# Kernel tuning notes

Hardware: AMD Instinct MI355X
Metric: run time of the kernel (lower is better)

## Reference

```python
import jax, jax.numpy as jnp
import numpy as np

EPS = 1e-5  # torch BatchNorm2d default eps

def _bn(x, gamma, beta):
    # training-mode batch statistics over (N,H,W), per channel (biased variance)
    mean = jnp.mean(x, axis=(0, 2, 3), keepdims=True)
    var = jnp.var(x, axis=(0, 2, 3), keepdims=True)
    return gamma[None, :, None, None] * (x - mean) * jax.lax.rsqrt(var + EPS) + beta[None, :, None, None]

def _conv1x1(x, w, b):
    # (B,C,H,W) x (O,C) -> (B,O,H,W)
    return jnp.einsum('bchw,oc->bohw', x, w) + b[None, :, None, None]

def _maxpool2(x):
    B, C, H, W = x.shape
    return x.reshape(B, C, H // 2, 2, W // 2, 2).max(axis=(3, 5))

def setup_inputs() -> dict:
    key = jax.random.key(0)
    ks = jax.random.split(key, 5)
    B, C, H, W = 16, 256, 56, 56
    Ci, Cg = C // 8, C // 4
    def kaiming(k, o, i):
        return jax.random.normal(k, (o, i), jnp.float32) * np.float32(np.sqrt(2.0 / i))
    return {
        'x': jax.random.normal(ks[0], (B, C, H, W), jnp.float32),
        'bn1_gamma': jnp.ones((C,), jnp.float32),
        'bn1_beta': jnp.zeros((C,), jnp.float32),
        'w_g': kaiming(ks[1], Cg, C), 'b_g': jnp.zeros((Cg,), jnp.float32),
        'w_theta': kaiming(ks[2], Ci, C), 'b_theta': jnp.zeros((Ci,), jnp.float32),
        'w_phi': kaiming(ks[3], Ci, C), 'b_phi': jnp.zeros((Ci,), jnp.float32),
        'bn2_gamma': jnp.ones((Cg,), jnp.float32),
        'bn2_beta': jnp.zeros((Cg,), jnp.float32),
        'w_z': kaiming(ks[4], C, Cg), 'b_z': jnp.zeros((C,), jnp.float32),
    }

def reference(x, bn1_gamma, bn1_beta, w_g, b_g, w_theta, b_theta, w_phi, b_phi, bn2_gamma, bn2_beta, w_z, b_z):
    identity = x
    B, C, H, W = x.shape
    xa = jax.nn.relu(_bn(x, bn1_gamma, bn1_beta))
    g_x = _maxpool2(_conv1x1(xa, w_g, b_g))        # (B,Cg,H/2,W/2)
    phi_x = _maxpool2(_conv1x1(xa, w_phi, b_phi))  # (B,Ci,H/2,W/2)
    theta_x = _conv1x1(xa, w_theta, b_theta)       # (B,Ci,H,W)
    Cg = g_x.shape[1]
    Ci = theta_x.shape[1]
    Np = g_x.shape[2] * g_x.shape[3]               # subsampled positions (H/2*W/2)
    g_x = g_x.reshape(B, Cg, Np).transpose(0, 2, 1)      # (B,Np,Cg)
    phi_x = phi_x.reshape(B, Ci, Np)                     # (B,Ci,Np)
    theta_x = theta_x.reshape(B, Ci, H * W).transpose(0, 2, 1)  # (B,HW,Ci)
    f_div_C = jnp.einsum('bnc,bcm->bnm', theta_x, phi_x) / Np   # (B,HW,Np)
    y = jnp.einsum('bnm,bmc->bnc', f_div_C, g_x)                # (B,HW,Cg)
    y = y.transpose(0, 2, 1).reshape(B, Cg, H, W)
    w_y = _conv1x1(jax.nn.relu(_bn(y, bn2_gamma, bn2_beta)), w_z, b_z)
    return w_y + identity
```

## Files before the change

kernel.cpp:

```cpp
#include <hip/hip_runtime.h>
#include <hip/hip_bf16.h>

#define BB 16
#define CC 256
#define HWN 3136
#define NCG 64
#define NCI 32
#define NPP 784

typedef __attribute__((ext_vector_type(8))) short short8;
typedef __attribute__((ext_vector_type(4))) float floatx4;

__device__ __forceinline__ unsigned short f2bf(float f) {
    union { __hip_bfloat16 h; unsigned short u; } cv;
    cv.h = __float2bfloat16(f);
    return cv.u;
}
__device__ __forceinline__ float bf2f(unsigned short u) {
    return __uint_as_float(((unsigned)u) << 16);
}

__global__ __launch_bounds__(256) void k_prep(const float* __restrict__ w_t,
                                              const float* __restrict__ w_p,
                                              const float* __restrict__ w_g,
                                              const float* __restrict__ w_z,
                                              unsigned short* __restrict__ wcat,
                                              unsigned short* __restrict__ wzb,
                                              unsigned short* __restrict__ pool,
                                              float* __restrict__ accs) {
    int o = blockIdx.x;
    int c = threadIdx.x;
    const float* src = (o < 32) ? (w_t + o * CC)
                      : (o < 64) ? (w_p + (o - 32) * CC)
                                 : (w_g + (o - 64) * CC);
    wcat[o * CC + c] = f2bf(src[c]);
    {
        int r = o * 2 + (c >> 7);
        int kk = c & 127;
        if (kk < 72)
            wzb[r * 72 + kk] = (kk < 64) ? f2bf(w_z[r * 64 + kk]) : (unsigned short)0;
    }
    if (o < 96) {
        int b = c >> 4, kk = c & 15;
        pool[((size_t)(b * 96 + o)) * 800 + 784 + kk] = 0;
    }
    if (o == 0) {
        for (int i = c; i < 640; i += 256) accs[i] = 0.f;
    }
}

__global__ __launch_bounds__(256) void k_bn1a(const float* __restrict__ x,
                                              float* __restrict__ acc) {
    int blk = blockIdx.x;
    int c = blk & (CC - 1);
    const float4* p = (const float4*)(x + (size_t)blk * HWN);
    int tid = threadIdx.x;
    float s = 0.f, q = 0.f;
    #pragma unroll
    for (int i = tid; i < 784; i += 256) {
        float4 v = p[i];
        s += v.x + v.y + v.z + v.w;
        q += v.x * v.x + v.y * v.y + v.z * v.z + v.w * v.w;
    }
    #pragma unroll
    for (int off = 32; off > 0; off >>= 1) {
        s += __shfl_down(s, off);
        q += __shfl_down(q, off);
    }
    __shared__ float sh[8];
    int wid = tid >> 6, lane = tid & 63;
    if (lane == 0) { sh[wid] = s; sh[4 + wid] = q; }
    __syncthreads();
    if (tid == 0) {
        atomicAdd(&acc[c], sh[0] + sh[1] + sh[2] + sh[3]);
        atomicAdd(&acc[CC + c], sh[4] + sh[5] + sh[6] + sh[7]);
    }
}

__global__ __launch_bounds__(256) void k_conv1(const float* __restrict__ x,
                                               const unsigned short* __restrict__ wcat,
                                               const float* __restrict__ bn1acc,
                                               const float* __restrict__ gamma,
                                               const float* __restrict__ beta,
                                               const float* __restrict__ b_g,
                                               const float* __restrict__ b_t,
                                               const float* __restrict__ b_p,
                                               unsigned short* __restrict__ th,
                                               unsigned short* __restrict__ pool) {
    int b  = blockIdx.y;
    int bx = blockIdx.x;
    int hw0 = bx * 112;
    int tid = threadIdx.x;
    int wv = tid >> 6, ln = tid & 63;
    int col = ln & 15, quad = ln >> 4;

    __shared__ unsigned short smem[128 * 120];
    unsigned short* As = smem;
    unsigned short* Bs = smem + 4096;
    __shared__ float ab_s[512];
    __shared__ float bias_s[128];

    {
        const float inv = 1.0f / (BB * HWN);
        float mean = bn1acc[tid] * inv;
        float var  = bn1acc[CC + tid] * inv - mean * mean;
        float a = gamma[tid] * rsqrtf(var + 1e-5f);
        ab_s[tid] = a;
        ab_s[CC + tid] = beta[tid] - mean * a;
    }
    if (tid < 128) {
        int o = tid;
        bias_s[o] = (o < 32) ? b_t[o] : (o < 64) ? b_p[o - 32] : b_g[o - 64];
    }
    __syncthreads();

    floatx4 acc[2][7];
    #pragma unroll
    for (int mt = 0; mt < 2; ++mt)
        for (int nt = 0; nt < 7; ++nt)
            acc[mt][nt] = (floatx4){0.f, 0.f, 0.f, 0.f};

    int p   = tid & 15;
    int hwq = tid >> 4;
    const float* xb = x + (size_t)(b * CC) * HWN + hw0;

    for (int k0 = 0; k0 < CC; k0 += 32) {
        #pragma unroll
        for (int i = 0; i < 2; ++i) {
            int row = wv * 32 + i * 16 + (ln >> 2);
            int q   = ln & 3;
            const unsigned short* gp = wcat + row * CC + k0 + q * 8;
            __builtin_amdgcn_global_load_lds(
                (const __attribute__((address_space(1))) unsigned int*)gp,
                (__attribute__((address_space(3))) unsigned int*)&As[(wv * 2 + i) * 512],
                16, 0, 0);
        }
        {
            int c0 = k0 + 2 * p;
            float a0 = ab_s[c0],     d0 = ab_s[CC + c0];
            float a1 = ab_s[c0 + 1], d1 = ab_s[CC + c0 + 1];
            unsigned int* bw = (unsigned int*)Bs;
            #pragma unroll
            for (int t = 0; t < 2; ++t) {
                int qi = hwq + 16 * t;
                if (qi < 28) {
                    float4 v0 = *(const float4*)(xb + (size_t)c0 * HWN + qi * 4);
                    float4 v1 = *(const float4*)(xb + (size_t)(c0 + 1) * HWN + qi * 4);
                    float r0[4] = { fmaxf(fmaf(a0, v0.x, d0), 0.f), fmaxf(fmaf(a0, v0.y, d0), 0.f),
                                    fmaxf(fmaf(a0, v0.z, d0), 0.f), fmaxf(fmaf(a0, v0.w, d0), 0.f) };
                    float r1[4] = { fmaxf(fmaf(a1, v1.x, d1), 0.f), fmaxf(fmaf(a1, v1.y, d1), 0.f),
                                    fmaxf(fmaf(a1, v1.z, d1), 0.f), fmaxf(fmaf(a1, v1.w, d1), 0.f) };
                    #pragma unroll
                    for (int i = 0; i < 4; ++i) {
                        unsigned int w = (unsigned int)f2bf(r0[i]) | ((unsigned int)f2bf(r1[i]) << 16);
                        bw[(qi * 4 + i) * 16 + p] = w;
                    }
                }
            }
        }
        __syncthreads();

        short8 af0 = *(const short8*)&As[(wv * 32 +      col) * 32 + quad * 8];
        short8 af1 = *(const short8*)&As[(wv * 32 + 16 + col) * 32 + quad * 8];
        #pragma unroll
        for (int nt = 0; nt < 7; ++nt) {
            short8 bf = *(const short8*)&Bs[(nt * 16 + col) * 32 + quad * 8];
            acc[0][nt] = __builtin_amdgcn_mfma_f32_16x16x32_bf16(af0, bf, acc[0][nt], 0, 0, 0);
            acc[1][nt] = __builtin_amdgcn_mfma_f32_16x16x32_bf16(af1, bf, acc[1][nt], 0, 0, 0);
        }
        __syncthreads();
    }

    unsigned short* Ct = smem;
    #pragma unroll
    for (int mt = 0; mt < 2; ++mt) {
        int obase = wv * 32 + mt * 16 + quad * 4;
        #pragma unroll
        for (int r = 0; r < 4; ++r) {
            float bias = bias_s[obase + r];
            #pragma unroll
            for (int nt = 0; nt < 7; ++nt)
                Ct[(obase + r) * 120 + nt * 16 + col] = f2bf(acc[mt][nt][r] + bias);
        }
    }
    __syncthreads();

    #pragma unroll
    for (int i = 0; i < 4; ++i) {
        int e = tid + i * 256;
        if (e < 896) {
            int ch = e / 28, c4 = e - ch * 28;
            ushort4 v = *(const ushort4*)&Ct[ch * 120 + c4 * 4];
            *(ushort4*)&th[((size_t)(b * NCI + ch)) * HWN + hw0 + c4 * 4] = v;
        }
    }
    #pragma unroll
    for (int i = 0; i < 11; ++i) {
        int e = tid + i * 256;
        if (e < 2688) {
            int ch = e / 28, m = e - ch * 28;
            const unsigned short* r0p = &Ct[(32 + ch) * 120 + 2 * m];
            float v = fmaxf(fmaxf(bf2f(r0p[0]), bf2f(r0p[1])),
                            fmaxf(bf2f(r0p[56]), bf2f(r0p[57])));
            pool[((size_t)(b * 96 + ch)) * 800 + bx * 28 + m] = f2bf(v);
        }
    }
}

__global__ __launch_bounds__(256) void k_sgemm(const unsigned short* __restrict__ pool,
                                               unsigned short* __restrict__ Sg) {
    int b = blockIdx.x;
    int tid = threadIdx.x;
    int wv = tid >> 6, ln = tid & 63;
    int col = ln & 15, quad = ln >> 4;
    __shared__ float Sred[4 * 2048];

    const unsigned short* gbase = pool + ((size_t)(b * 96 + 32)) * 800;
    const unsigned short* pbase = pool + ((size_t)(b * 96)) * 800;

    floatx4 acc[4][2];
    #pragma unroll
    for (int mt = 0; mt < 4; ++mt)
        for (int nt = 0; nt < 2; ++nt)
            acc[mt][nt] = (floatx4){0.f, 0.f, 0.f, 0.f};

    for (int s = wv; s < 25; s += 4) {
        int k0 = s * 32;
        short8 af[4], bfr[2];
        #pragma unroll
        for (int mt = 0; mt < 4; ++mt)
            af[mt] = *(const short8*)&gbase[(mt * 16 + col) * 800 + k0 + quad * 8];
        #pragma unroll
        for (int nt = 0; nt < 2; ++nt)
            bfr[nt] = *(const short8*)&pbase[(nt * 16 + col) * 800 + k0 + quad * 8];
        #pragma unroll
        for (int mt = 0; mt < 4; ++mt)
            #pragma unroll
            for (int nt = 0; nt < 2; ++nt)
                acc[mt][nt] = __builtin_amdgcn_mfma_f32_16x16x32_bf16(af[mt], bfr[nt], acc[mt][nt], 0, 0, 0);
    }
    #pragma unroll
    for (int mt = 0; mt < 4; ++mt)
        for (int nt = 0; nt < 2; ++nt)
            for (int r = 0; r < 4; ++r) {
                int cg = mt * 16 + quad * 4 + r;
                int ci = nt * 16 + col;
                Sred[wv * 2048 + cg * 32 + ci] = acc[mt][nt][r];
            }
    __syncthreads();
    #pragma unroll
    for (int j = 0; j < 8; ++j) {
        int idx = tid + j * 256;
        float s = Sred[idx] + Sred[2048 + idx] + Sred[4096 + idx] + Sred[6144 + idx];
        int cg = idx >> 5, ci = idx & 31;
        Sg[(size_t)b * 2560 + cg * 40 + ci] = f2bf(s * (1.0f / NPP));
    }
}

__global__ __launch_bounds__(256) void k_y(const unsigned short* __restrict__ th,
                                           const unsigned short* __restrict__ Sg,
                                           unsigned short* __restrict__ y,
                                           float* __restrict__ bn2acc) {
    int b = blockIdx.y;
    int hw0 = blockIdx.x * 64;
    int tid = threadIdx.x;
    int wv = tid >> 6, ln = tid & 63;
    int col = ln & 15, quad = ln >> 4;

    __shared__ unsigned short St[64 * 40];
    __shared__ unsigned short Tt[64 * 40];
    __shared__ float shs[64], shq[64];

    {
        const unsigned int* sgw = (const unsigned int*)(Sg + (size_t)b * 2560);
        unsigned int* stw = (unsigned int*)St;
        for (int i = tid; i < 1280; i += 256) stw[i] = sgw[i];
    }
    {
        int p2 = tid & 15, hwq = tid >> 4;
        int c0 = 2 * p2;
        const unsigned short* tb = th + (size_t)(b * NCI) * HWN + hw0 + hwq * 4;
        ushort4 v0 = *(const ushort4*)(tb + (size_t)c0 * HWN);
        ushort4 v1 = *(const ushort4*)(tb + (size_t)(c0 + 1) * HWN);
        unsigned int* tw = (unsigned int*)Tt;
        tw[(hwq * 4 + 0) * 20 + p2] = (unsigned)v0.x | ((unsigned)v1.x << 16);
        tw[(hwq * 4 + 1) * 20 + p2] = (unsigned)v0.y | ((unsigned)v1.y << 16);
        tw[(hwq * 4 + 2) * 20 + p2] = (unsigned)v0.z | ((unsigned)v1.z << 16);
        tw[(hwq * 4 + 3) * 20 + p2] = (unsigned)v0.w | ((unsigned)v1.w << 16);
    }
    if (tid < 64) { shs[tid] = 0.f; shq[tid] = 0.f; }
    __syncthreads();

    short8 af = *(const short8*)&Tt[(wv * 16 + col) * 40 + quad * 8];
    #pragma unroll
    for (int nt = 0; nt < 4; ++nt) {
        short8 bf = *(const short8*)&St[(nt * 16 + col) * 40 + quad * 8];
        floatx4 acc = (floatx4){0.f, 0.f, 0.f, 0.f};
        acc = __builtin_amdgcn_mfma_f32_16x16x32_bf16(af, bf, acc, 0, 0, 0);
        int cg = nt * 16 + col;
        int hw = hw0 + wv * 16 + quad * 4;
        ushort4 st;
        st.x = f2bf(acc[0]); st.y = f2bf(acc[1]);
        st.z = f2bf(acc[2]); st.w = f2bf(acc[3]);
        *(ushort4*)&y[((size_t)(b * NCG + cg)) * HWN + hw] = st;
        float s = acc[0] + acc[1] + acc[2] + acc[3];
        float q = acc[0] * acc[0] + acc[1] * acc[1] + acc[2] * acc[2] + acc[3] * acc[3];
        atomicAdd(&shs[cg], s);
        atomicAdd(&shq[cg], q);
    }
    __syncthreads();
    if (tid < 64) {
        atomicAdd(&bn2acc[tid], shs[tid]);
        atomicAdd(&bn2acc[64 + tid], shq[tid]);
    }
}

__global__ __launch_bounds__(256) void k_convz(const unsigned short* __restrict__ y,
                                               const unsigned short* __restrict__ wzb,
                                               const float* __restrict__ bn2acc,
                                               const float* __restrict__ gamma,
                                               const float* __restrict__ beta,
                                               const float* __restrict__ b_z,
                                               const float* __restrict__ x,
                                               float* __restrict__ out) {
    int b = blockIdx.y;
    int hw0 = blockIdx.x * 64;
    int tid = threadIdx.x;
    int wv = tid >> 6, ln = tid & 63;
    int col = ln & 15, quad = ln >> 4;

    __shared__ unsigned short Wl[256 * 72];
    __shared__ unsigned short Yt[64 * 72];
    __shared__ float ab2_s[128];

    #pragma unroll
    for (int i = 0; i < 9; ++i) {
        int j = wv * 9 + i;
        const unsigned short* gp = wzb + j * 512 + ln * 8;
        __builtin_amdgcn_global_load_lds(
            (const __attribute__((address_space(1))) unsigned int*)gp,
            (__attribute__((address_space(3))) unsigned int*)&Wl[j * 512],
            16, 0, 0);
    }
    if (tid < 64) {
        const float inv = 1.0f / (BB * HWN);
        float mean = bn2acc[tid] * inv;
        float var  = bn2acc[64 + tid] * inv - mean * mean;
        float a = gamma[tid] * rsqrtf(var + 1e-5f);
        ab2_s[tid] = a;
        ab2_s[64 + tid] = beta[tid] - mean * a;
    }
    __syncthreads();

    {
        int p2 = tid & 15, hwq = tid >> 4;
        const unsigned short* ybase = y + (size_t)(b * NCG) * HWN + hw0 + hwq * 4;
        unsigned int* yw = (unsigned int*)Yt;
        #pragma unroll
        for (int h = 0; h < 2; ++h) {
            int k0 = h * 32 + 2 * p2;
            ushort4 v0 = *(const ushort4*)(ybase + (size_t)k0 * HWN);
            ushort4 v1 = *(const ushort4*)(ybase + (size_t)(k0 + 1) * HWN);
            float a0 = ab2_s[k0],     d0 = ab2_s[64 + k0];
            float a1 = ab2_s[k0 + 1], d1 = ab2_s[64 + k0 + 1];
            float r0[4] = { fmaxf(fmaf(a0, bf2f(v0.x), d0), 0.f), fmaxf(fmaf(a0, bf2f(v0.y), d0), 0.f),
                            fmaxf(fmaf(a0, bf2f(v0.z), d0), 0.f), fmaxf(fmaf(a0, bf2f(v0.w), d0), 0.f) };
            float r1[4] = { fmaxf(fmaf(a1, bf2f(v1.x), d1), 0.f), fmaxf(fmaf(a1, bf2f(v1.y), d1), 0.f),
                            fmaxf(fmaf(a1, bf2f(v1.z), d1), 0.f), fmaxf(fmaf(a1, bf2f(v1.w), d1), 0.f) };
            #pragma unroll
            for (int i = 0; i < 4; ++i) {
                unsigned int w = (unsigned int)f2bf(r0[i]) | ((unsigned int)f2bf(r1[i]) << 16);
                yw[(hwq * 4 + i) * 36 + h * 16 + p2] = w;
            }
        }
    }
    __syncthreads();

    floatx4 acc[16];
    #pragma unroll
    for (int nt = 0; nt < 16; ++nt) acc[nt] = (floatx4){0.f, 0.f, 0.f, 0.f};

    #pragma unroll
    for (int kk = 0; kk < 2; ++kk) {
        short8 af = *(const short8*)&Yt[(wv * 16 + col) * 72 + kk * 32 + quad * 8];
        #pragma unroll
        for (int nt = 0; nt < 16; ++nt) {
            short8 bf = *(const short8*)&Wl[(nt * 16 + col) * 72 + kk * 32 + quad * 8];
            acc[nt] = __builtin_amdgcn_mfma_f32_16x16x32_bf16(af, bf, acc[nt], 0, 0, 0);
        }
    }

    #pragma unroll
    for (int nt = 0; nt < 16; ++nt) {
        int co = nt * 16 + col;
        size_t base = ((size_t)(b * CC + co)) * HWN + hw0 + wv * 16 + quad * 4;
        float4 xv = *(const float4*)&x[base];
        float bz = b_z[co];
        float4 r = make_float4(acc[nt][0] + bz + xv.x, acc[nt][1] + bz + xv.y,
                               acc[nt][2] + bz + xv.z, acc[nt][3] + bz + xv.w);
        *(float4*)&out[base] = r;
    }
}

extern "C" void kernel_launch(void* const* d_in, const int* in_sizes, int n_in,
                              void* d_out, int out_size, void* d_ws, size_t ws_size,
                              hipStream_t stream) {
    (void)in_sizes; (void)n_in; (void)out_size; (void)ws_size;
    const float* x   = (const float*)d_in[0];
    const float* g1  = (const float*)d_in[1];
    const float* b1  = (const float*)d_in[2];
    const float* w_g = (const float*)d_in[3];
    const float* b_g = (const float*)d_in[4];
    const float* w_t = (const float*)d_in[5];
    const float* b_t = (const float*)d_in[6];
    const float* w_p = (const float*)d_in[7];
    const float* b_p = (const float*)d_in[8];
    const float* g2  = (const float*)d_in[9];
    const float* b2  = (const float*)d_in[10];
    const float* w_z = (const float*)d_in[11];
    const float* b_z = (const float*)d_in[12];
    float* out = (float*)d_out;

    float* ws     = (float*)d_ws;
    float* bn1acc = ws;
    float* bn2acc = ws + 512;
    unsigned short* wcat  = (unsigned short*)(ws + 1024);
    unsigned short* wzb   = (unsigned short*)(ws + 17408);
    unsigned short* th    = (unsigned short*)(ws + 26624);
    unsigned short* pool  = (unsigned short*)(ws + 829440);
    unsigned short* Sg    = (unsigned short*)(ws + 1443840);
    unsigned short* yb    = (unsigned short*)(ws + 1464320);

    k_prep  <<<dim3(128),     dim3(256), 0, stream>>>(w_t, w_p, w_g, w_z, wcat, wzb, pool, ws);
    k_bn1a  <<<dim3(BB * CC), dim3(256), 0, stream>>>(x, bn1acc);
    k_conv1 <<<dim3(28, BB),  dim3(256), 0, stream>>>(x, wcat, bn1acc, g1, b1, b_g, b_t, b_p, th, pool);
    k_sgemm <<<dim3(BB),      dim3(256), 0, stream>>>(pool, Sg);
    k_y     <<<dim3(49, BB),  dim3(256), 0, stream>>>(th, Sg, yb, bn2acc);
    k_convz <<<dim3(49, BB),  dim3(256), 0, stream>>>(yb, wzb, bn2acc, g2, b2, b_z, x, out);
}
```

Baseline: 192.8 us.

## Derive BN2 statistics algebraically from theta Gram matrix and fuse y into convz

Instead of materialising y and accumulating its BN2 statistics in a separate kernel, the per-channel sum and sum-of-squares of y are computed from theta row sums and the theta Gram matrix combined with the small S matrix inside k_sgemm. k_y is removed and y is recomputed on the fly in k_convz, which is also split over two output-channel halves. conv1 additionally prefetches the next x chunk into registers. This removes a full write and read of the y tensor, at the cost of extra Gram work in the 16-block sgemm kernel and y being recomputed twice per tile in convz.

```diff
diff --git a/kernel.cpp b/kernel.cpp
--- a/kernel.cpp
+++ b/kernel.cpp
@@ -45,7 +45,7 @@
         pool[((size_t)(b * 96 + o)) * 800 + 784 + kk] = 0;
     }
     if (o == 0) {
-        for (int i = c; i < 640; i += 256) accs[i] = 0.f;
+        for (int i = c; i < 1152; i += 256) accs[i] = 0.f;
     }
 }
 
@@ -86,7 +86,8 @@
                                                const float* __restrict__ b_t,
                                                const float* __restrict__ b_p,
                                                unsigned short* __restrict__ th,
-                                               unsigned short* __restrict__ pool) {
+                                               unsigned short* __restrict__ pool,
+                                               float* __restrict__ T1g) {
     int b  = blockIdx.y;
     int bx = blockIdx.x;
     int hw0 = bx * 112;
@@ -123,6 +124,18 @@
     int p   = tid & 15;
     int hwq = tid >> 4;
     const float* xb = x + (size_t)(b * CC) * HWN + hw0;
+    bool q1 = (hwq + 16) < 28;
+
+    float4 pv0[2], pv1[2];
+    {
+        int c0 = 2 * p;
+        pv0[0] = *(const float4*)(xb + (size_t)c0 * HWN + hwq * 4);
+        pv1[0] = *(const float4*)(xb + (size_t)(c0 + 1) * HWN + hwq * 4);
+        if (q1) {
+            pv0[1] = *(const float4*)(xb + (size_t)c0 * HWN + (hwq + 16) * 4);
+            pv1[1] = *(const float4*)(xb + (size_t)(c0 + 1) * HWN + (hwq + 16) * 4);
+        }
+    }
 
     for (int k0 = 0; k0 < CC; k0 += 32) {
         #pragma unroll
@@ -142,10 +155,9 @@
             unsigned int* bw = (unsigned int*)Bs;
             #pragma unroll
             for (int t = 0; t < 2; ++t) {
-                int qi = hwq + 16 * t;
-                if (qi < 28) {
-                    float4 v0 = *(const float4*)(xb + (size_t)c0 * HWN + qi * 4);
-                    float4 v1 = *(const float4*)(xb + (size_t)(c0 + 1) * HWN + qi * 4);
+                if (t == 0 || q1) {
+                    int qi = hwq + 16 * t;
+                    float4 v0 = pv0[t], v1 = pv1[t];
                     float r0[4] = { fmaxf(fmaf(a0, v0.x, d0), 0.f), fmaxf(fmaf(a0, v0.y, d0), 0.f),
                                     fmaxf(fmaf(a0, v0.z, d0), 0.f), fmaxf(fmaf(a0, v0.w, d0), 0.f) };
                     float r1[4] = { fmaxf(fmaf(a1, v1.x, d1), 0.f), fmaxf(fmaf(a1, v1.y, d1), 0.f),
@@ -158,6 +170,15 @@
                 }
             }
         }
+        if (k0 + 32 < CC) {
+            int c0 = k0 + 32 + 2 * p;
+            pv0[0] = *(const float4*)(xb + (size_t)c0 * HWN + hwq * 4);
+            pv1[0] = *(const float4*)(xb + (size_t)(c0 + 1) * HWN + hwq * 4);
+            if (q1) {
+                pv0[1] = *(const float4*)(xb + (size_t)c0 * HWN + (hwq + 16) * 4);
+                pv1[1] = *(const float4*)(xb + (size_t)(c0 + 1) * HWN + (hwq + 16) * 4);
+            }
+        }
         __syncthreads();
 
         short8 af0 = *(const short8*)&As[(wv * 32 +      col) * 32 + quad * 8];
@@ -193,6 +214,17 @@
             ushort4 v = *(const ushort4*)&Ct[ch * 120 + c4 * 4];
             *(ushort4*)&th[((size_t)(b * NCI + ch)) * HWN + hw0 + c4 * 4] = v;
         }
+    }
+    {
+        int row = tid >> 3;
+        int seg = tid & 7;
+        float s = 0.f;
+        #pragma unroll
+        for (int j = 0; j < 14; ++j) s += bf2f(Ct[row * 120 + seg * 14 + j]);
+        s += __shfl_down(s, 4);
+        s += __shfl_down(s, 2);
+        s += __shfl_down(s, 1);
+        if (seg == 0) atomicAdd(&T1g[b * NCI + row], s);
     }
     #pragma unroll
     for (int i = 0; i < 11; ++i) {
@@ -207,70 +239,153 @@
     }
 }
 
-__global__ __launch_bounds__(256) void k_sgemm(const unsigned short* __restrict__ pool,
-                                               unsigned short* __restrict__ Sg) {
+__global__ __launch_bounds__(512) void k_sgemm(const unsigned short* __restrict__ pool,
+                                               const unsigned short* __restrict__ th,
+                                               const float* __restrict__ T1g,
+                                               unsigned short* __restrict__ Sg,
+                                               float* __restrict__ bn2acc) {
     int b = blockIdx.x;
     int tid = threadIdx.x;
     int wv = tid >> 6, ln = tid & 63;
     int col = ln & 15, quad = ln >> 4;
     __shared__ float Sred[4 * 2048];
-
-    const unsigned short* gbase = pool + ((size_t)(b * 96 + 32)) * 800;
-    const unsigned short* pbase = pool + ((size_t)(b * 96)) * 800;
-
-    floatx4 acc[4][2];
-    #pragma unroll
-    for (int mt = 0; mt < 4; ++mt)
-        for (int nt = 0; nt < 2; ++nt)
-            acc[mt][nt] = (floatx4){0.f, 0.f, 0.f, 0.f};
-
-    for (int s = wv; s < 25; s += 4) {
-        int k0 = s * 32;
-        short8 af[4], bfr[2];
+    __shared__ float Gred[4 * 1024];
+    __shared__ float T1s[32];
+    __shared__ float shs[64], shq[64];
+
+    if (tid < 64) { shs[tid] = 0.f; shq[tid] = 0.f; }
+    if (tid < 32) T1s[tid] = T1g[b * NCI + tid];
+
+    if (wv < 4) {
+        const unsigned short* gbase = pool + ((size_t)(b * 96 + 32)) * 800;
+        const unsigned short* pbase = pool + ((size_t)(b * 96)) * 800;
+        floatx4 acc[4][2];
         #pragma unroll
         for (int mt = 0; mt < 4; ++mt)
-            af[mt] = *(const short8*)&gbase[(mt * 16 + col) * 800 + k0 + quad * 8];
-        #pragma unroll
-        for (int nt = 0; nt < 2; ++nt)
-            bfr[nt] = *(const short8*)&pbase[(nt * 16 + col) * 800 + k0 + quad * 8];
+            for (int nt = 0; nt < 2; ++nt)
+                acc[mt][nt] = (floatx4){0.f, 0.f, 0.f, 0.f};
+        for (int s = wv; s < 25; s += 4) {
+            int k0 = s * 32;
+            short8 af[4], bfr[2];
+            #pragma unroll
+            for (int mt = 0; mt < 4; ++mt)
+                af[mt] = *(const short8*)&gbase[(mt * 16 + col) * 800 + k0 + quad * 8];
+            #pragma unroll
+            for (int nt = 0; nt < 2; ++nt)
+                bfr[nt] = *(const short8*)&pbase[(nt * 16 + col) * 800 + k0 + quad * 8];
+            #pragma unroll
+            for (int mt = 0; mt < 4; ++mt)
+                #pragma unroll
+                for (int nt = 0; nt < 2; ++nt)
+                    acc[mt][nt] = __builtin_amdgcn_mfma_f32_16x16x32_bf16(af[mt], bfr[nt], acc[mt][nt], 0, 0, 0);
+        }
         #pragma unroll
         for (int mt = 0; mt < 4; ++mt)
-            #pragma unroll
             for (int nt = 0; nt < 2; ++nt)
-                acc[mt][nt] = __builtin_amdgcn_mfma_f32_16x16x32_bf16(af[mt], bfr[nt], acc[mt][nt], 0, 0, 0);
-    }
-    #pragma unroll
-    for (int mt = 0; mt < 4; ++mt)
-        for (int nt = 0; nt < 2; ++nt)
-            for (int r = 0; r < 4; ++r) {
-                int cg = mt * 16 + quad * 4 + r;
-                int ci = nt * 16 + col;
-                Sred[wv * 2048 + cg * 32 + ci] = acc[mt][nt][r];
-            }
-    __syncthreads();
-    #pragma unroll
-    for (int j = 0; j < 8; ++j) {
-        int idx = tid + j * 256;
+                for (int r = 0; r < 4; ++r) {
+                    int cg = mt * 16 + quad * 4 + r;
+                    int ci = nt * 16 + col;
+                    Sred[wv * 2048 + cg * 32 + ci] = acc[mt][nt][r];
+                }
+    } else {
+        int gw = wv - 4;
+        const unsigned short* tb = th + (size_t)(b * NCI) * HWN;
+        floatx4 ga[2][2];
+        #pragma unroll
+        for (int m = 0; m < 2; ++m)
+            for (int n = 0; n < 2; ++n)
+                ga[m][n] = (floatx4){0.f, 0.f, 0.f, 0.f};
+        for (int t = gw; t < 98; t += 4) {
+            int k0 = t * 32;
+            short8 a0 = *(const short8*)&tb[(size_t)col * HWN + k0 + quad * 8];
+            short8 a1 = *(const short8*)&tb[(size_t)(16 + col) * HWN + k0 + quad * 8];
+            ga[0][0] = __builtin_amdgcn_mfma_f32_16x16x32_bf16(a0, a0, ga[0][0], 0, 0, 0);
+            ga[0][1] = __builtin_amdgcn_mfma_f32_16x16x32_bf16(a0, a1, ga[0][1], 0, 0, 0);
+            ga[1][0] = __builtin_amdgcn_mfma_f32_16x16x32_bf16(a1, a0, ga[1][0], 0, 0, 0);
+            ga[1][1] = __builtin_amdgcn_mfma_f32_16x16x32_bf16(a1, a1, ga[1][1], 0, 0, 0);
+        }
+        #pragma unroll
+        for (int m = 0; m < 2; ++m)
+            for (int n = 0; n < 2; ++n)
+                for (int r = 0; r < 4; ++r)
+                    Gred[gw * 1024 + (m * 16 + quad * 4 + r) * 32 + n * 16 + col] = ga[m][n][r];
+    }
+    __syncthreads();
+
+    for (int idx = tid; idx < 2048; idx += 512) {
         float s = Sred[idx] + Sred[2048 + idx] + Sred[4096 + idx] + Sred[6144 + idx];
         int cg = idx >> 5, ci = idx & 31;
-        Sg[(size_t)b * 2560 + cg * 40 + ci] = f2bf(s * (1.0f / NPP));
-    }
-}
-
-__global__ __launch_bounds__(256) void k_y(const unsigned short* __restrict__ th,
-                                           const unsigned short* __restrict__ Sg,
-                                           unsigned short* __restrict__ y,
-                                           float* __restrict__ bn2acc) {
+        unsigned short h = f2bf(s * (1.0f / NPP));
+        Sg[(size_t)b * 2560 + cg * 40 + ci] = h;
+        Sred[idx] = bf2f(h);
+    }
+    for (int idx = tid; idx < 1024; idx += 512) {
+        Gred[idx] = Gred[idx] + Gred[1024 + idx] + Gred[2048 + idx] + Gred[3072 + idx];
+    }
+    __syncthreads();
+
+    {
+        int cg = tid & 63, part = tid >> 6;
+        float sum = 0.f, sq = 0.f;
+        #pragma unroll
+        for (int i = 0; i < 4; ++i) {
+            int ci = part * 4 + i;
+            float sv = Sred[cg * 32 + ci];
+            sum += sv * T1s[ci];
+            float t = 0.f;
+            #pragma unroll
+            for (int cj = 0; cj < 32; ++cj)
+                t += Gred[ci * 32 + cj] * Sred[cg * 32 + cj];
+            sq += sv * t;
+        }
+        atomicAdd(&shs[cg], sum);
+        atomicAdd(&shq[cg], sq);
+    }
+    __syncthreads();
+    if (tid < 64) {
+        atomicAdd(&bn2acc[tid], shs[tid]);
+        atomicAdd(&bn2acc[64 + tid], shq[tid]);
+    }
+}
+
+__global__ __launch_bounds__(256) void k_convz(const unsigned short* __restrict__ th,
+                                               const unsigned short* __restrict__ Sg,
+                                               const unsigned short* __restrict__ wzb,
+                                               const float* __restrict__ bn2acc,
+                                               const float* __restrict__ gamma,
+                                               const float* __restrict__ beta,
+                                               const float* __restrict__ b_z,
+                                               const float* __restrict__ x,
+                                               float* __restrict__ out) {
     int b = blockIdx.y;
     int hw0 = blockIdx.x * 64;
+    int coh = blockIdx.z * 128;
     int tid = threadIdx.x;
     int wv = tid >> 6, ln = tid & 63;
     int col = ln & 15, quad = ln >> 4;
 
-    __shared__ unsigned short St[64 * 40];
-    __shared__ unsigned short Tt[64 * 40];
-    __shared__ float shs[64], shq[64];
-
+    __shared__ unsigned short Wl[128 * 72];
+    __shared__ unsigned short TS[5120];
+    __shared__ float ab2_s[128];
+    unsigned short* Tt = TS;
+    unsigned short* St = TS + 2560;
+    unsigned short* Yt = TS;
+
+    for (int j = wv; j < 18; j += 4) {
+        const unsigned short* gp = wzb + coh * 72 + j * 512 + ln * 8;
+        __builtin_amdgcn_global_load_lds(
+            (const __attribute__((address_space(1))) unsigned int*)gp,
+            (__attribute__((address_space(3))) unsigned int*)&Wl[j * 512],
+            16, 0, 0);
+    }
+    if (tid < 64) {
+        const float inv = 1.0f / (BB * HWN);
+        float mean = bn2acc[tid] * inv;
+        float var  = bn2acc[64 + tid] * inv - mean * mean;
+        float a = gamma[tid] * rsqrtf(var + 1e-5f);
+        ab2_s[tid] = a;
+        ab2_s[64 + tid] = beta[tid] - mean * a;
+    }
     {
         const unsigned int* sgw = (const unsigned int*)(Sg + (size_t)b * 2560);
         unsigned int* stw = (unsigned int*)St;
@@ -288,111 +403,47 @@
         tw[(hwq * 4 + 2) * 20 + p2] = (unsigned)v0.z | ((unsigned)v1.z << 16);
         tw[(hwq * 4 + 3) * 20 + p2] = (unsigned)v0.w | ((unsigned)v1.w << 16);
     }
-    if (tid < 64) { shs[tid] = 0.f; shq[tid] = 0.f; }
-    __syncthreads();
-
-    short8 af = *(const short8*)&Tt[(wv * 16 + col) * 40 + quad * 8];
+    __syncthreads();
+
+    short8 afy = *(const short8*)&Tt[(wv * 16 + col) * 40 + quad * 8];
+    floatx4 yacc[4];
     #pragma unroll
     for (int nt = 0; nt < 4; ++nt) {
         short8 bf = *(const short8*)&St[(nt * 16 + col) * 40 + quad * 8];
-        floatx4 acc = (floatx4){0.f, 0.f, 0.f, 0.f};
-        acc = __builtin_amdgcn_mfma_f32_16x16x32_bf16(af, bf, acc, 0, 0, 0);
+        floatx4 z = (floatx4){0.f, 0.f, 0.f, 0.f};
+        yacc[nt] = __builtin_amdgcn_mfma_f32_16x16x32_bf16(afy, bf, z, 0, 0, 0);
+    }
+    __syncthreads();
+
+    #pragma unroll
+    for (int nt = 0; nt < 4; ++nt) {
         int cg = nt * 16 + col;
-        int hw = hw0 + wv * 16 + quad * 4;
-        ushort4 st;
-        st.x = f2bf(acc[0]); st.y = f2bf(acc[1]);
-        st.z = f2bf(acc[2]); st.w = f2bf(acc[3]);
-        *(ushort4*)&y[((size_t)(b * NCG + cg)) * HWN + hw] = st;
-        float s = acc[0] + acc[1] + acc[2] + acc[3];
-        float q = acc[0] * acc[0] + acc[1] * acc[1] + acc[2] * acc[2] + acc[3] * acc[3];
-        atomicAdd(&shs[cg], s);
-        atomicAdd(&shq[cg], q);
-    }
-    __syncthreads();
-    if (tid < 64) {
-        atomicAdd(&bn2acc[tid], shs[tid]);
-        atomicAdd(&bn2acc[64 + tid], shq[tid]);
-    }
-}
-
-__global__ __launch_bounds__(256) void k_convz(const unsigned short* __restrict__ y,
-                                               const unsigned short* __restrict__ wzb,
-                                               const float* __restrict__ bn2acc,
-                                               const float* __restrict__ gamma,
-                                               const float* __restrict__ beta,
-                                               const float* __restrict__ b_z,
-                                               const float* __restrict__ x,
-                                               float* __restrict__ out) {
-    int b = blockIdx.y;
-    int hw0 = blockIdx.x * 64;
-    int tid = threadIdx.x;
-    int wv = tid >> 6, ln = tid & 63;
-    int col = ln & 15, quad = ln >> 4;
-
-    __shared__ unsigned short Wl[256 * 72];
-    __shared__ unsigned short Yt[64 * 72];
-    __shared__ float ab2_s[128];
-
-    #pragma unroll
-    for (int i = 0; i < 9; ++i) {
-        int j = wv * 9 + i;
-        const unsigned short* gp = wzb + j * 512 + ln * 8;
-        __builtin_amdgcn_global_load_lds(
-            (const __attribute__((address_space(1))) unsigned int*)gp,
-            (__attribute__((address_space(3))) unsigned int*)&Wl[j * 512],
-            16, 0, 0);
-    }
-    if (tid < 64) {
-        const float inv = 1.0f / (BB * HWN);
-        float mean = bn2acc[tid] * inv;
-        float var  = bn2acc[64 + tid] * inv - mean * mean;
-        float a = gamma[tid] * rsqrtf(var + 1e-5f);
-        ab2_s[tid] = a;
-        ab2_s[64 + tid] = beta[tid] - mean * a;
-    }
-    __syncthreads();
-
-    {
-        int p2 = tid & 15, hwq = tid >> 4;
-        const unsigned short* ybase = y + (size_t)(b * NCG) * HWN + hw0 + hwq * 4;
-        unsigned int* yw = (unsigned int*)Yt;
-        #pragma unroll
-        for (int h = 0; h < 2; ++h) {
-            int k0 = h * 32 + 2 * p2;
-            ushort4 v0 = *(const ushort4*)(ybase + (size_t)k0 * HWN);
-            ushort4 v1 = *(const ushort4*)(ybase + (size_t)(k0 + 1) * HWN);
-            float a0 = ab2_s[k0],     d0 = ab2_s[64 + k0];
-            float a1 = ab2_s[k0 + 1], d1 = ab2_s[64 + k0 + 1];
-            float r0[4] = { fmaxf(fmaf(a0, bf2f(v0.x), d0), 0.f), fmaxf(fmaf(a0, bf2f(v0.y), d0), 0.f),
-                            fmaxf(fmaf(a0, bf2f(v0.z), d0), 0.f), fmaxf(fmaf(a0, bf2f(v0.w), d0), 0.f) };
-            float r1[4] = { fmaxf(fmaf(a1, bf2f(v1.x), d1), 0.f), fmaxf(fmaf(a1, bf2f(v1.y), d1), 0.f),
-                            fmaxf(fmaf(a1, bf2f(v1.z), d1), 0.f), fmaxf(fmaf(a1, bf2f(v1.w), d1), 0.f) };
-            #pragma unroll
-            for (int i = 0; i < 4; ++i) {
-                unsigned int w = (unsigned int)f2bf(r0[i]) | ((unsigned int)f2bf(r1[i]) << 16);
-                yw[(hwq * 4 + i) * 36 + h * 16 + p2] = w;
-            }
-        }
-    }
-    __syncthreads();
-
-    floatx4 acc[16];
-    #pragma unroll
-    for (int nt = 0; nt < 16; ++nt) acc[nt] = (floatx4){0.f, 0.f, 0.f, 0.f};
+        float a = ab2_s[cg], d = ab2_s[64 + cg];
+        #pragma unroll
+        for (int r = 0; r < 4; ++r) {
+            int hwl = wv * 16 + quad * 4 + r;
+            Yt[hwl * 72 + cg] = f2bf(fmaxf(fmaf(a, yacc[nt][r], d), 0.f));
+        }
+    }
+    __syncthreads();
+
+    floatx4 acc[8];
+    #pragma unroll
+    for (int nt = 0; nt < 8; ++nt) acc[nt] = (floatx4){0.f, 0.f, 0.f, 0.f};
 
     #pragma unroll
     for (int kk = 0; kk < 2; ++kk) {
-        short8 af = *(const short8*)&Yt[(wv * 16 + col) * 72 + kk * 32 + quad * 8];
-        #pragma unroll
-        for (int nt = 0; nt < 16; ++nt) {
+        short8 afm = *(const short8*)&Yt[(wv * 16 + col) * 72 + kk * 32 + quad * 8];
+        #pragma unroll
+        for (int nt = 0; nt < 8; ++nt) {
             short8 bf = *(const short8*)&Wl[(nt * 16 + col) * 72 + kk * 32 + quad * 8];
-            acc[nt] = __builtin_amdgcn_mfma_f32_16x16x32_bf16(af, bf, acc[nt], 0, 0, 0);
-        }
-    }
-
-    #pragma unroll
-    for (int nt = 0; nt < 16; ++nt) {
-        int co = nt * 16 + col;
+            acc[nt] = __builtin_amdgcn_mfma_f32_16x16x32_bf16(afm, bf, acc[nt], 0, 0, 0);
+        }
+    }
+
+    #pragma unroll
+    for (int nt = 0; nt < 8; ++nt) {
+        int co = coh + nt * 16 + col;
         size_t base = ((size_t)(b * CC + co)) * HWN + hw0 + wv * 16 + quad * 4;
         float4 xv = *(const float4*)&x[base];
         float bz = b_z[co];
@@ -424,17 +475,16 @@
     float* ws     = (float*)d_ws;
     float* bn1acc = ws;
     float* bn2acc = ws + 512;
-    unsigned short* wcat  = (unsigned short*)(ws + 1024);
-    unsigned short* wzb   = (unsigned short*)(ws + 17408);
-    unsigned short* th    = (unsigned short*)(ws + 26624);
-    unsigned short* pool  = (unsigned short*)(ws + 829440);
-    unsigned short* Sg    = (unsigned short*)(ws + 1443840);
-    unsigned short* yb    = (unsigned short*)(ws + 1464320);
-
-    k_prep  <<<dim3(128),     dim3(256), 0, stream>>>(w_t, w_p, w_g, w_z, wcat, wzb, pool, ws);
-    k_bn1a  <<<dim3(BB * CC), dim3(256), 0, stream>>>(x, bn1acc);
-    k_conv1 <<<dim3(28, BB),  dim3(256), 0, stream>>>(x, wcat, bn1acc, g1, b1, b_g, b_t, b_p, th, pool);
-    k_sgemm <<<dim3(BB),      dim3(256), 0, stream>>>(pool, Sg);
-    k_y     <<<dim3(49, BB),  dim3(256), 0, stream>>>(th, Sg, yb, bn2acc);
-    k_convz <<<dim3(49, BB),  dim3(256), 0, stream>>>(yb, wzb, bn2acc, g2, b2, b_z, x, out);
-}
+    float* T1g    = ws + 640;
+    unsigned short* wcat = (unsigned short*)(ws + 1152);
+    unsigned short* wzb  = (unsigned short*)(ws + 17536);
+    unsigned short* th   = (unsigned short*)(ws + 26752);
+    unsigned short* pool = (unsigned short*)(ws + 829568);
+    unsigned short* Sg   = (unsigned short*)(ws + 1443968);
+
+    k_prep  <<<dim3(128),        dim3(256), 0, stream>>>(w_t, w_p, w_g, w_z, wcat, wzb, pool, ws);
+    k_bn1a  <<<dim3(BB * CC),    dim3(256), 0, stream>>>(x, bn1acc);
+    k_conv1 <<<dim3(28, BB),     dim3(256), 0, stream>>>(x, wcat, bn1acc, g1, b1, b_g, b_t, b_p, th, pool, T1g);
+    k_sgemm <<<dim3(BB),         dim3(512), 0, stream>>>(pool, th, T1g, Sg, bn2acc);
+    k_convz <<<dim3(49, BB, 2),  dim3(256), 0, stream>>>(th, Sg, wzb, bn2acc, g2, b2, b_z, x, out);
+}
```

After: 173.8 us. -9.9%, faster.
